# Performance work log

Measured on AMD Instinct MI355X. Metric: run time of the kernel, lower is better.

## Reference

```python
import jax, jax.numpy as jnp
import numpy as np

B, H, S, D, C = 8, 8, 1024, 64, 21

def setup_inputs() -> dict:
    key = jax.random.key(0)
    ks = jax.random.split(key, 7)
    return {
        "Q": jax.random.normal(ks[0], (B, H, S, D), dtype=jnp.float32),
        "K": jax.random.normal(ks[1], (B, H, S, D), dtype=jnp.float32),
        "V": jax.random.normal(ks[2], (B, H, S, D), dtype=jnp.float32),
        "dtw_cost": jax.random.normal(ks[3], (B, C, S, S), dtype=jnp.float32),
        "mask": jax.random.randint(ks[4], (B, 1, S, S), 0, 2, dtype=jnp.int32),
        "W": jax.random.normal(ks[5], (H, C), dtype=jnp.float32) * 0.1,
        "b": jax.random.normal(ks[6], (H,), dtype=jnp.float32) * 0.1,
    }

def reference(Q, K, V, dtw_cost, mask, W, b):
    d_k = Q.shape[-1]
    # scores: [B,H,S,S]
    scores = jnp.einsum("bhqd,bhkd->bhqk", Q, K) / jnp.sqrt(jnp.float32(d_k))
    # Linear over DTW-cost channel dim, producing per-head bias [B,H,S,S]
    # (equivalent to permute -> nn.Linear -> permute in the torch code)
    bias = jnp.einsum("bcqk,hc->bhqk", dtw_cost, W) + b[None, :, None, None]
    scores = scores + bias
    scores = jnp.where(mask == 0, jnp.float32(-1e9), scores)
    attention = jax.nn.softmax(scores, axis=-1)
    output = jnp.einsum("bhqk,bhkd->bhqd", attention, V)
    return (output, attention)
```

## Files before the change

### kernel.cpp

```cpp
#include <hip/hip_runtime.h>
#include <stdint.h>

#define Bq 8
#define Hh 8
#define Ss 1024
#define Dd 64
#define Cc 21

typedef short bf16x8 __attribute__((ext_vector_type(8)));
typedef float f32x4 __attribute__((ext_vector_type(4)));

__device__ __forceinline__ unsigned short f2bf(float f) {
  union { float f; uint32_t u; } v; v.f = f;
  uint32_t u = v.u;
  u += 0x7FFFu + ((u >> 16) & 1u);
  return (unsigned short)(u >> 16);
}

__global__ __launch_bounds__(256) void bias_kernel(
    const float* __restrict__ dtw, const int* __restrict__ mask,
    const float* __restrict__ W, const float* __restrict__ bv,
    float* __restrict__ attn) {
  __shared__ float sW[Hh * Cc];
  __shared__ float sb[Hh];
  int t = threadIdx.x;
  if (t < Hh * Cc) sW[t] = W[t];
  if (t < Hh) sb[t] = bv[t];
  __syncthreads();
  int b = blockIdx.x >> 10;
  int q = blockIdx.x & 1023;
  int k = t << 2;
  size_t dbase = (((size_t)b * Cc) * Ss + q) * Ss + k;
  float acc[Hh][4];
#pragma unroll
  for (int h = 0; h < Hh; ++h) {
    float bb = sb[h];
    acc[h][0] = bb; acc[h][1] = bb; acc[h][2] = bb; acc[h][3] = bb;
  }
  for (int c = 0; c < Cc; ++c) {
    float4 dv = *(const float4*)(dtw + dbase + (size_t)c * Ss * Ss);
#pragma unroll
    for (int h = 0; h < Hh; ++h) {
      float w = sW[h * Cc + c];
      acc[h][0] += w * dv.x; acc[h][1] += w * dv.y;
      acc[h][2] += w * dv.z; acc[h][3] += w * dv.w;
    }
  }
  int4 mv = *(const int4*)(mask + ((size_t)b * Ss + q) * Ss + k);
#pragma unroll
  for (int h = 0; h < Hh; ++h) {
    float4 o;
    o.x = (mv.x == 0) ? -1e9f : acc[h][0];
    o.y = (mv.y == 0) ? -1e9f : acc[h][1];
    o.z = (mv.z == 0) ? -1e9f : acc[h][2];
    o.w = (mv.w == 0) ? -1e9f : acc[h][3];
    *(float4*)(attn + ((((size_t)b * Hh + h) * Ss + q) * Ss + k)) = o;
  }
}

__global__ __launch_bounds__(256) void attn_kernel(
    const float* __restrict__ Q, const float* __restrict__ K,
    const float* __restrict__ V, float* __restrict__ out,
    float* __restrict__ attn) {
  __shared__ unsigned short qtile[32][72];
  __shared__ unsigned short kvt[64][72];
  __shared__ float red[4][16];
  __shared__ float linv[32];
  __shared__ float omerge[32][64];

  int t = threadIdx.x;
  int w = t >> 6;
  int lane = t & 63;
  int quad = lane >> 4;
  int l16 = lane & 15;

  int qt = blockIdx.x & 31;
  int bh = blockIdx.x >> 5;
  int q0 = qt << 5;

  const float* Qp = Q + ((size_t)bh * Ss + q0) * Dd;
  const float* Kp = K + (size_t)bh * Ss * Dd;
  const float* Vp = V + (size_t)bh * Ss * Dd;
  float* attp = attn + (size_t)bh * Ss * Ss + (size_t)q0 * Ss;
  float* outp = out + ((size_t)bh * Ss + q0) * Dd;

  {
    int row = t >> 3;
    int col = (t & 7) << 3;
    float4 a = *(const float4*)(Qp + row * Dd + col);
    float4 b2 = *(const float4*)(Qp + row * Dd + col + 4);
    qtile[row][col + 0] = f2bf(a.x * 0.125f);
    qtile[row][col + 1] = f2bf(a.y * 0.125f);
    qtile[row][col + 2] = f2bf(a.z * 0.125f);
    qtile[row][col + 3] = f2bf(a.w * 0.125f);
    qtile[row][col + 4] = f2bf(b2.x * 0.125f);
    qtile[row][col + 5] = f2bf(b2.y * 0.125f);
    qtile[row][col + 6] = f2bf(b2.z * 0.125f);
    qtile[row][col + 7] = f2bf(b2.w * 0.125f);
  }

  int mt = w & 1;
  int ntb = (w >> 1) << 1;
  int mrow = mt * 16 + l16;
  float lsum[4] = {0.f, 0.f, 0.f, 0.f};

  for (int kt = 0; kt < 16; ++kt) {
    int k0 = kt << 6;
    __syncthreads();
    {
      int row = t >> 2;
      int colb = (t & 3) << 4;
#pragma unroll
      for (int i = 0; i < 4; ++i) {
        float4 v4 = *(const float4*)(Kp + (size_t)(k0 + row) * Dd + colb + i * 4);
        kvt[row][colb + i * 4 + 0] = f2bf(v4.x);
        kvt[row][colb + i * 4 + 1] = f2bf(v4.y);
        kvt[row][colb + i * 4 + 2] = f2bf(v4.z);
        kvt[row][colb + i * 4 + 3] = f2bf(v4.w);
      }
    }
    __syncthreads();
#pragma unroll
    for (int nti = 0; nti < 2; ++nti) {
      int nt = ntb + nti;
      f32x4 acc = {0.f, 0.f, 0.f, 0.f};
#pragma unroll
      for (int ks = 0; ks < 2; ++ks) {
        bf16x8 af = *(const bf16x8*)&qtile[mrow][ks * 32 + quad * 8];
        bf16x8 bfr = *(const bf16x8*)&kvt[nt * 16 + l16][ks * 32 + quad * 8];
        acc = __builtin_amdgcn_mfma_f32_16x16x32_bf16(af, bfr, acc, 0, 0, 0);
      }
      int kcol = k0 + nt * 16 + l16;
      int rb = mt * 16 + quad * 4;
#pragma unroll
      for (int r = 0; r < 4; ++r) {
        float* sp = attp + (size_t)(rb + r) * Ss + kcol;
        float sc = acc[r] + *sp;
        *sp = sc;
        lsum[r] += __expf(sc);
      }
    }
  }
#pragma unroll
  for (int off = 1; off < 16; off <<= 1) {
#pragma unroll
    for (int r = 0; r < 4; ++r) lsum[r] += __shfl_xor(lsum[r], off, 64);
  }
  if (l16 == 0) {
#pragma unroll
    for (int r = 0; r < 4; ++r) red[w][quad * 4 + r] = lsum[r];
  }
  __syncthreads();
  if (t < 32) {
    int mtt = t >> 4, rl = t & 15;
    linv[t] = 1.0f / (red[mtt][rl] + red[mtt + 2][rl]);
  }
  __syncthreads();

  int par = w >> 1;
  float li = linv[mrow];
  f32x4 oacc[4];
#pragma unroll
  for (int dt = 0; dt < 4; ++dt) {
    oacc[dt][0] = 0.f; oacc[dt][1] = 0.f; oacc[dt][2] = 0.f; oacc[dt][3] = 0.f;
  }
  for (int it = 0; it < 16; ++it) {
    int k0 = it << 6;
    __syncthreads();
    {
      int row = t >> 2;
      int colb = (t & 3) << 4;
#pragma unroll
      for (int i = 0; i < 4; ++i) {
        float4 v4 = *(const float4*)(Vp + (size_t)(k0 + row) * Dd + colb + i * 4);
        kvt[colb + i * 4 + 0][row] = f2bf(v4.x);
        kvt[colb + i * 4 + 1][row] = f2bf(v4.y);
        kvt[colb + i * 4 + 2][row] = f2bf(v4.z);
        kvt[colb + i * 4 + 3][row] = f2bf(v4.w);
      }
    }
    __syncthreads();
    int ks = k0 + par * 32;
    float* sp = attp + (size_t)mrow * Ss + ks + quad * 8;
    float4 s0 = *(const float4*)sp;
    float4 s1 = *(const float4*)(sp + 4);
    float p0 = __expf(s0.x) * li, p1 = __expf(s0.y) * li;
    float p2 = __expf(s0.z) * li, p3 = __expf(s0.w) * li;
    float p4 = __expf(s1.x) * li, p5 = __expf(s1.y) * li;
    float p6 = __expf(s1.z) * li, p7 = __expf(s1.w) * li;
    *(float4*)sp = make_float4(p0, p1, p2, p3);
    *(float4*)(sp + 4) = make_float4(p4, p5, p6, p7);
    bf16x8 af;
    af[0] = (short)f2bf(p0); af[1] = (short)f2bf(p1);
    af[2] = (short)f2bf(p2); af[3] = (short)f2bf(p3);
    af[4] = (short)f2bf(p4); af[5] = (short)f2bf(p5);
    af[6] = (short)f2bf(p6); af[7] = (short)f2bf(p7);
#pragma unroll
    for (int dt = 0; dt < 4; ++dt) {
      bf16x8 bfr = *(const bf16x8*)&kvt[dt * 16 + l16][par * 32 + quad * 8];
      oacc[dt] = __builtin_amdgcn_mfma_f32_16x16x32_bf16(af, bfr, oacc[dt], 0, 0, 0);
    }
  }
  __syncthreads();
  if (par == 0) {
#pragma unroll
    for (int dt = 0; dt < 4; ++dt)
#pragma unroll
      for (int r = 0; r < 4; ++r)
        omerge[mt * 16 + quad * 4 + r][dt * 16 + l16] = oacc[dt][r];
  }
  __syncthreads();
  if (par == 1) {
#pragma unroll
    for (int dt = 0; dt < 4; ++dt)
#pragma unroll
      for (int r = 0; r < 4; ++r)
        omerge[mt * 16 + quad * 4 + r][dt * 16 + l16] += oacc[dt][r];
  }
  __syncthreads();
  {
    int row = t >> 3;
    int col = (t & 7) << 3;
    float4 o0 = *(const float4*)&omerge[row][col];
    float4 o1 = *(const float4*)&omerge[row][col + 4];
    *(float4*)(outp + row * Dd + col) = o0;
    *(float4*)(outp + row * Dd + col + 4) = o1;
  }
}

extern "C" void kernel_launch(void* const* d_in, const int* in_sizes, int n_in,
                              void* d_out, int out_size, void* d_ws, size_t ws_size,
                              hipStream_t stream) {
  const float* Q = (const float*)d_in[0];
  const float* K = (const float*)d_in[1];
  const float* V = (const float*)d_in[2];
  const float* dtw = (const float*)d_in[3];
  const int* mask = (const int*)d_in[4];
  const float* W = (const float*)d_in[5];
  const float* bv = (const float*)d_in[6];
  float* out = (float*)d_out;
  float* attn = out + (size_t)Bq * Hh * Ss * Dd;

  bias_kernel<<<Bq * Ss, 256, 0, stream>>>(dtw, mask, W, bv, attn);
  attn_kernel<<<Bq * Hh * (Ss / 32), 256, 0, stream>>>(Q, K, V, out, attn);
}
```

Measured before the change: 1.323 ms.

## Fuse DTW bias projection with QK^T scoring and exp into one kernel

```diff
diff --git a/kernel.cpp b/kernel.cpp
--- a/kernel.cpp
+++ b/kernel.cpp
@@ -17,54 +17,163 @@
   return (unsigned short)(u >> 16);
 }
 
-__global__ __launch_bounds__(256) void bias_kernel(
+__device__ __forceinline__ bf16x8 pack8(float4 a, float4 b) {
+  bf16x8 f;
+  f[0] = (short)f2bf(a.x); f[1] = (short)f2bf(a.y);
+  f[2] = (short)f2bf(a.z); f[3] = (short)f2bf(a.w);
+  f[4] = (short)f2bf(b.x); f[5] = (short)f2bf(b.y);
+  f[6] = (short)f2bf(b.z); f[7] = (short)f2bf(b.w);
+  return f;
+}
+
+__global__ __launch_bounds__(512) void score_kernel(
+    const float* __restrict__ Q, const float* __restrict__ K,
     const float* __restrict__ dtw, const int* __restrict__ mask,
     const float* __restrict__ W, const float* __restrict__ bv,
-    float* __restrict__ attn) {
-  __shared__ float sW[Hh * Cc];
+    float* __restrict__ attn, float* __restrict__ lpart) {
+  __shared__ float sBias[Hh][32][33];
+  __shared__ float sWT[Cc][Hh];
   __shared__ float sb[Hh];
+
+  const size_t SS = (size_t)Ss * Ss;
   int t = threadIdx.x;
-  if (t < Hh * Cc) sW[t] = W[t];
+  if (t < Hh * Cc) { int h = t / Cc; int c = t - h * Cc; sWT[c][h] = W[t]; }
   if (t < Hh) sb[t] = bv[t];
-  __syncthreads();
-  int b = blockIdx.x >> 10;
-  int q = blockIdx.x & 1023;
-  int k = t << 2;
-  size_t dbase = (((size_t)b * Cc) * Ss + q) * Ss + k;
-  float acc[Hh][4];
-#pragma unroll
-  for (int h = 0; h < Hh; ++h) {
-    float bb = sb[h];
-    acc[h][0] = bb; acc[h][1] = bb; acc[h][2] = bb; acc[h][3] = bb;
-  }
-  for (int c = 0; c < Cc; ++c) {
-    float4 dv = *(const float4*)(dtw + dbase + (size_t)c * Ss * Ss);
-#pragma unroll
-    for (int h = 0; h < Hh; ++h) {
-      float w = sW[h * Cc + c];
-      acc[h][0] += w * dv.x; acc[h][1] += w * dv.y;
-      acc[h][2] += w * dv.z; acc[h][3] += w * dv.w;
+
+  int kc  = blockIdx.x & 3;
+  int qt  = (blockIdx.x >> 2) & 31;
+  int b   = blockIdx.x >> 7;
+  int q0  = qt << 5;
+  int kc0 = kc << 8;
+
+  int w = t >> 6;
+  int lane = t & 63;
+  int quad = lane >> 4;
+  int l16 = lane & 15;
+  size_t bh = (size_t)b * Hh + w;
+
+  bf16x8 qa[2][2];
+  {
+    const float* Qbase = Q + (bh * Ss + q0) * Dd;
+#pragma unroll
+    for (int mt = 0; mt < 2; ++mt)
+#pragma unroll
+      for (int ks = 0; ks < 2; ++ks) {
+        const float* qp = Qbase + (mt * 16 + l16) * Dd + ks * 32 + quad * 8;
+        float4 x = *(const float4*)qp;
+        float4 y = *(const float4*)(qp + 4);
+        x.x *= 0.125f; x.y *= 0.125f; x.z *= 0.125f; x.w *= 0.125f;
+        y.x *= 0.125f; y.y *= 0.125f; y.z *= 0.125f; y.w *= 0.125f;
+        qa[mt][ks] = pack8(x, y);
+      }
+  }
+
+  const float* Kbase = K + (bh * Ss + kc0) * Dd;
+  const float* dbase = dtw + (size_t)b * Cc * SS + (size_t)q0 * Ss + kc0;
+  const int* mbase = mask + ((size_t)b * Ss + q0) * Ss + kc0;
+  float* attp = attn + (bh * Ss + q0) * Ss + kc0;
+
+  int qr = t >> 5;
+  int kcell = t & 31;
+
+  float lsum[2][4];
+#pragma unroll
+  for (int mt = 0; mt < 2; ++mt)
+#pragma unroll
+    for (int r = 0; r < 4; ++r) lsum[mt][r] = 0.f;
+
+  for (int kt = 0; kt < 8; ++kt) {
+    int k0 = kt << 5;
+    float4 kf[8];
+#pragma unroll
+    for (int nt = 0; nt < 2; ++nt)
+#pragma unroll
+      for (int ks = 0; ks < 2; ++ks) {
+        const float* kp =
+            Kbase + (size_t)(k0 + nt * 16 + l16) * Dd + ks * 32 + quad * 8;
+        kf[(nt * 2 + ks) * 2 + 0] = *(const float4*)kp;
+        kf[(nt * 2 + ks) * 2 + 1] = *(const float4*)(kp + 4);
+      }
+    __syncthreads();
+    {
+      const float* dp0 = dbase + (size_t)qr * Ss + k0 + kcell;
+      const float* dp1 = dp0 + (size_t)16 * Ss;
+      float a0[8], a1[8];
+#pragma unroll
+      for (int h = 0; h < 8; ++h) { a0[h] = sb[h]; a1[h] = sb[h]; }
+#pragma unroll
+      for (int c = 0; c < Cc; ++c) {
+        float v0 = *dp0; dp0 += SS;
+        float v1 = *dp1; dp1 += SS;
+        float4 wa = *(const float4*)&sWT[c][0];
+        float4 wb = *(const float4*)&sWT[c][4];
+        a0[0] += wa.x * v0; a0[1] += wa.y * v0;
+        a0[2] += wa.z * v0; a0[3] += wa.w * v0;
+        a0[4] += wb.x * v0; a0[5] += wb.y * v0;
+        a0[6] += wb.z * v0; a0[7] += wb.w * v0;
+        a1[0] += wa.x * v1; a1[1] += wa.y * v1;
+        a1[2] += wa.z * v1; a1[3] += wa.w * v1;
+        a1[4] += wb.x * v1; a1[5] += wb.y * v1;
+        a1[6] += wb.z * v1; a1[7] += wb.w * v1;
+      }
+      int m0 = mbase[(size_t)qr * Ss + k0 + kcell];
+      int m1 = mbase[(size_t)(qr + 16) * Ss + k0 + kcell];
+#pragma unroll
+      for (int h = 0; h < 8; ++h) {
+        sBias[h][qr][kcell] = m0 ? a0[h] : -1e9f;
+        sBias[h][qr + 16][kcell] = m1 ? a1[h] : -1e9f;
+      }
     }
-  }
-  int4 mv = *(const int4*)(mask + ((size_t)b * Ss + q) * Ss + k);
-#pragma unroll
-  for (int h = 0; h < Hh; ++h) {
-    float4 o;
-    o.x = (mv.x == 0) ? -1e9f : acc[h][0];
-    o.y = (mv.y == 0) ? -1e9f : acc[h][1];
-    o.z = (mv.z == 0) ? -1e9f : acc[h][2];
-    o.w = (mv.w == 0) ? -1e9f : acc[h][3];
-    *(float4*)(attn + ((((size_t)b * Hh + h) * Ss + q) * Ss + k)) = o;
-  }
-}
-
-__global__ __launch_bounds__(256) void attn_kernel(
-    const float* __restrict__ Q, const float* __restrict__ K,
+    __syncthreads();
+    bf16x8 kb[2][2];
+#pragma unroll
+    for (int nt = 0; nt < 2; ++nt)
+#pragma unroll
+      for (int ks = 0; ks < 2; ++ks)
+        kb[nt][ks] = pack8(kf[(nt * 2 + ks) * 2], kf[(nt * 2 + ks) * 2 + 1]);
+    f32x4 acc[2][2];
+#pragma unroll
+    for (int mt = 0; mt < 2; ++mt)
+#pragma unroll
+      for (int nt = 0; nt < 2; ++nt) {
+        f32x4 a = {0.f, 0.f, 0.f, 0.f};
+        a = __builtin_amdgcn_mfma_f32_16x16x32_bf16(qa[mt][0], kb[nt][0], a, 0, 0, 0);
+        a = __builtin_amdgcn_mfma_f32_16x16x32_bf16(qa[mt][1], kb[nt][1], a, 0, 0, 0);
+        acc[mt][nt] = a;
+      }
+#pragma unroll
+    for (int mt = 0; mt < 2; ++mt)
+#pragma unroll
+      for (int nt = 0; nt < 2; ++nt)
+#pragma unroll
+        for (int r = 0; r < 4; ++r) {
+          int lrow = mt * 16 + quad * 4 + r;
+          float s = acc[mt][nt][r] + sBias[w][lrow][nt * 16 + l16];
+          float p = __expf(s);
+          lsum[mt][r] += p;
+          attp[(size_t)lrow * Ss + k0 + nt * 16 + l16] = p;
+        }
+  }
+#pragma unroll
+  for (int off = 1; off < 16; off <<= 1)
+#pragma unroll
+    for (int mt = 0; mt < 2; ++mt)
+#pragma unroll
+      for (int r = 0; r < 4; ++r)
+        lsum[mt][r] += __shfl_xor(lsum[mt][r], off, 64);
+  if (l16 == 0) {
+#pragma unroll
+    for (int mt = 0; mt < 2; ++mt)
+#pragma unroll
+      for (int r = 0; r < 4; ++r)
+        lpart[(bh * Ss + q0 + mt * 16 + quad * 4 + r) * Dd + kc] = lsum[mt][r];
+  }
+}
+
+__global__ __launch_bounds__(256) void pv_kernel(
     const float* __restrict__ V, float* __restrict__ out,
     float* __restrict__ attn) {
-  __shared__ unsigned short qtile[32][72];
-  __shared__ unsigned short kvt[64][72];
-  __shared__ float red[4][16];
+  __shared__ unsigned short vt[Dd][72];
   __shared__ float linv[32];
   __shared__ float omerge[32][64];
 
@@ -75,119 +184,51 @@
   int l16 = lane & 15;
 
   int qt = blockIdx.x & 31;
-  int bh = blockIdx.x >> 5;
+  size_t bh = blockIdx.x >> 5;
   int q0 = qt << 5;
 
-  const float* Qp = Q + ((size_t)bh * Ss + q0) * Dd;
-  const float* Kp = K + (size_t)bh * Ss * Dd;
-  const float* Vp = V + (size_t)bh * Ss * Dd;
-  float* attp = attn + (size_t)bh * Ss * Ss + (size_t)q0 * Ss;
-  float* outp = out + ((size_t)bh * Ss + q0) * Dd;
-
-  {
-    int row = t >> 3;
-    int col = (t & 7) << 3;
-    float4 a = *(const float4*)(Qp + row * Dd + col);
-    float4 b2 = *(const float4*)(Qp + row * Dd + col + 4);
-    qtile[row][col + 0] = f2bf(a.x * 0.125f);
-    qtile[row][col + 1] = f2bf(a.y * 0.125f);
-    qtile[row][col + 2] = f2bf(a.z * 0.125f);
-    qtile[row][col + 3] = f2bf(a.w * 0.125f);
-    qtile[row][col + 4] = f2bf(b2.x * 0.125f);
-    qtile[row][col + 5] = f2bf(b2.y * 0.125f);
-    qtile[row][col + 6] = f2bf(b2.z * 0.125f);
-    qtile[row][col + 7] = f2bf(b2.w * 0.125f);
-  }
+  const float* Vp = V + bh * Ss * Dd;
+  float* attp = attn + (bh * Ss + q0) * Ss;
+  float* outp = out + (bh * Ss + q0) * Dd;
+
+  if (t < 32) {
+    float4 lp = *(const float4*)(outp + t * Dd);
+    linv[t] = 1.0f / (lp.x + lp.y + lp.z + lp.w);
+  }
+  __syncthreads();
 
   int mt = w & 1;
-  int ntb = (w >> 1) << 1;
+  int par = w >> 1;
   int mrow = mt * 16 + l16;
-  float lsum[4] = {0.f, 0.f, 0.f, 0.f};
-
-  for (int kt = 0; kt < 16; ++kt) {
-    int k0 = kt << 6;
+  float li = linv[mrow];
+
+  f32x4 oacc[4];
+#pragma unroll
+  for (int dt = 0; dt < 4; ++dt) {
+    oacc[dt][0] = 0.f; oacc[dt][1] = 0.f; oacc[dt][2] = 0.f; oacc[dt][3] = 0.f;
+  }
+
+  for (int it = 0; it < 16; ++it) {
+    int k0 = it << 6;
     __syncthreads();
     {
       int row = t >> 2;
       int colb = (t & 3) << 4;
 #pragma unroll
       for (int i = 0; i < 4; ++i) {
-        float4 v4 = *(const float4*)(Kp + (size_t)(k0 + row) * Dd + colb + i * 4);
-        kvt[row][colb + i * 4 + 0] = f2bf(v4.x);
-        kvt[row][colb + i * 4 + 1] = f2bf(v4.y);
-        kvt[row][colb + i * 4 + 2] = f2bf(v4.z);
-        kvt[row][colb + i * 4 + 3] = f2bf(v4.w);
+        float4 v4 = *(const float4*)(Vp + (size_t)(k0 + row) * Dd + colb + i * 4);
+        vt[colb + i * 4 + 0][row] = f2bf(v4.x);
+        vt[colb + i * 4 + 1][row] = f2bf(v4.y);
+        vt[colb + i * 4 + 2][row] = f2bf(v4.z);
+        vt[colb + i * 4 + 3][row] = f2bf(v4.w);
       }
     }
     __syncthreads();
-#pragma unroll
-    for (int nti = 0; nti < 2; ++nti) {
-      int nt = ntb + nti;
-      f32x4 acc = {0.f, 0.f, 0.f, 0.f};
-#pragma unroll
-      for (int ks = 0; ks < 2; ++ks) {
-        bf16x8 af = *(const bf16x8*)&qtile[mrow][ks * 32 + quad * 8];
-        bf16x8 bfr = *(const bf16x8*)&kvt[nt * 16 + l16][ks * 32 + quad * 8];
-        acc = __builtin_amdgcn_mfma_f32_16x16x32_bf16(af, bfr, acc, 0, 0, 0);
-      }
-      int kcol = k0 + nt * 16 + l16;
-      int rb = mt * 16 + quad * 4;
-#pragma unroll
-      for (int r = 0; r < 4; ++r) {
-        float* sp = attp + (size_t)(rb + r) * Ss + kcol;
-        float sc = acc[r] + *sp;
-        *sp = sc;
-        lsum[r] += __expf(sc);
-      }
-    }
-  }
-#pragma unroll
-  for (int off = 1; off < 16; off <<= 1) {
-#pragma unroll
-    for (int r = 0; r < 4; ++r) lsum[r] += __shfl_xor(lsum[r], off, 64);
-  }
-  if (l16 == 0) {
-#pragma unroll
-    for (int r = 0; r < 4; ++r) red[w][quad * 4 + r] = lsum[r];
-  }
-  __syncthreads();
-  if (t < 32) {
-    int mtt = t >> 4, rl = t & 15;
-    linv[t] = 1.0f / (red[mtt][rl] + red[mtt + 2][rl]);
-  }
-  __syncthreads();
-
-  int par = w >> 1;
-  float li = linv[mrow];
-  f32x4 oacc[4];
-#pragma unroll
-  for (int dt = 0; dt < 4; ++dt) {
-    oacc[dt][0] = 0.f; oacc[dt][1] = 0.f; oacc[dt][2] = 0.f; oacc[dt][3] = 0.f;
-  }
-  for (int it = 0; it < 16; ++it) {
-    int k0 = it << 6;
-    __syncthreads();
-    {
-      int row = t >> 2;
-      int colb = (t & 3) << 4;
-#pragma unroll
-      for (int i = 0; i < 4; ++i) {
-        float4 v4 = *(const float4*)(Vp + (size_t)(k0 + row) * Dd + colb + i * 4);
-        kvt[colb + i * 4 + 0][row] = f2bf(v4.x);
-        kvt[colb + i * 4 + 1][row] = f2bf(v4.y);
-        kvt[colb + i * 4 + 2][row] = f2bf(v4.z);
-        kvt[colb + i * 4 + 3][row] = f2bf(v4.w);
-      }
-    }
-    __syncthreads();
-    int ks = k0 + par * 32;
-    float* sp = attp + (size_t)mrow * Ss + ks + quad * 8;
+    float* sp = attp + (size_t)mrow * Ss + k0 + par * 32 + quad * 8;
     float4 s0 = *(const float4*)sp;
     float4 s1 = *(const float4*)(sp + 4);
-    float p0 = __expf(s0.x) * li, p1 = __expf(s0.y) * li;
-    float p2 = __expf(s0.z) * li, p3 = __expf(s0.w) * li;
-    float p4 = __expf(s1.x) * li, p5 = __expf(s1.y) * li;
-    float p6 = __expf(s1.z) * li, p7 = __expf(s1.w) * li;
+    float p0 = s0.x * li, p1 = s0.y * li, p2 = s0.z * li, p3 = s0.w * li;
+    float p4 = s1.x * li, p5 = s1.y * li, p6 = s1.z * li, p7 = s1.w * li;
     *(float4*)sp = make_float4(p0, p1, p2, p3);
     *(float4*)(sp + 4) = make_float4(p4, p5, p6, p7);
     bf16x8 af;
@@ -197,7 +238,7 @@
     af[6] = (short)f2bf(p6); af[7] = (short)f2bf(p7);
 #pragma unroll
     for (int dt = 0; dt < 4; ++dt) {
-      bf16x8 bfr = *(const bf16x8*)&kvt[dt * 16 + l16][par * 32 + quad * 8];
+      bf16x8 bfr = *(const bf16x8*)&vt[dt * 16 + l16][par * 32 + quad * 8];
       oacc[dt] = __builtin_amdgcn_mfma_f32_16x16x32_bf16(af, bfr, oacc[dt], 0, 0, 0);
     }
   }
@@ -241,6 +282,6 @@
   float* out = (float*)d_out;
   float* attn = out + (size_t)Bq * Hh * Ss * Dd;
 
-  bias_kernel<<<Bq * Ss, 256, 0, stream>>>(dtw, mask, W, bv, attn);
-  attn_kernel<<<Bq * Hh * (Ss / 32), 256, 0, stream>>>(Q, K, V, out, attn);
-}
+  score_kernel<<<Bq * 32 * 4, 512, 0, stream>>>(Q, K, dtw, mask, W, bv, attn, out);
+  pv_kernel<<<Bq * Hh * (Ss / 32), 256, 0, stream>>>(V, out, attn);
+}
```

After: 1.249 ms. 5.6% less time.
